# Performance work log

Hardware: AMD Instinct MI355X
Metric: run time of the kernel (lower is better)

Reference implementation:

```python
import jax, jax.numpy as jnp
import numpy as np

B, C, H, W = 4, 64, 128, 128
NUM_HEAD = 1
SCALE = (C // NUM_HEAD) ** (-0.5)


def setup_inputs():
    key = jax.random.key(0)
    ks = jax.random.split(key, 32)
    def nrm(k, shape, s=0.05):
        return jax.random.normal(k, shape, jnp.float32) * s
    inp = {"x": jax.random.normal(ks[0], (B, C, H, W), jnp.float32)}
    i = 1
    for wn, bn in [("Wq", "bq"), ("Wk", "bk"), ("Wv", "bv"), ("Wl", "bl"), ("Wo", "bo"), ("Wp", "bp")]:
        inp[wn] = nrm(ks[i], (C, C)); i += 1
        inp[bn] = nrm(ks[i], (C,)); i += 1
    inp["sch_dw"] = nrm(ks[i], (C, 1, 5, 1)); i += 1
    inp["sch_dwb"] = nrm(ks[i], (C,)); i += 1
    inp["sch_pw"] = nrm(ks[i], (C, C, 1, 1)); i += 1
    inp["sch_pwb"] = nrm(ks[i], (C,)); i += 1
    inp["scv_dw"] = nrm(ks[i], (C, 1, 1, 5)); i += 1
    inp["scv_dwb"] = nrm(ks[i], (C,)); i += 1
    inp["scv_pw"] = nrm(ks[i], (C, C, 1, 1)); i += 1
    inp["scv_pwb"] = nrm(ks[i], (C,)); i += 1
    inp["convh_w"] = nrm(ks[i], (C, C, 1, 1)); i += 1
    inp["convh_b"] = nrm(ks[i], (C,)); i += 1
    inp["dsc_dw"] = nrm(ks[i], (C, 1, 3, 3)); i += 1
    inp["dsc_dwb"] = nrm(ks[i], (C,)); i += 1
    inp["dsc_pw"] = nrm(ks[i], (C, C, 1, 1)); i += 1
    inp["dsc_pwb"] = nrm(ks[i], (C,)); i += 1
    inp["ln_g"] = jnp.ones((C,), jnp.float32)
    inp["ln_b"] = jnp.zeros((C,), jnp.float32)
    return inp


def _linear(x, w, b):  # x [B,N,C], w [C,C] (torch Linear convention: y = x @ w.T + b)
    return x @ w.T + b


def _dwconv(x, w, b, pad):  # depthwise: x [B,C,H,W], w [C,1,kh,kw]
    y = jax.lax.conv_general_dilated(x, w, (1, 1), [(pad[0], pad[0]), (pad[1], pad[1])],
                                     dimension_numbers=("NCHW", "OIHW", "NCHW"),
                                     feature_group_count=x.shape[1])
    return y + b[None, :, None, None]


def _pwconv(x, w, b):  # 1x1 conv: w [Co,Ci,1,1]
    return jnp.einsum("bchw,oc->bohw", x, w[:, :, 0, 0]) + b[None, :, None, None]


def _attn(q, k, v):  # [B,N,C] each; dense NxN softmax attention
    a = jax.nn.softmax(jnp.einsum("bnc,bmc->bnm", q, k) * SCALE, axis=-1)
    return jnp.einsum("bnm,bmc->bnc", a, v)


def _up2_bilinear(x):  # bilinear, scale 2, align_corners=True
    Bb, Cc, Hh, Ww = x.shape
    def coords(n):
        s = jnp.linspace(0.0, n - 1.0, 2 * n)
        i0 = jnp.floor(s).astype(jnp.int32)
        i1 = jnp.minimum(i0 + 1, n - 1)
        return i0, i1, (s - i0).astype(x.dtype)
    y0, y1, wy = coords(Hh)
    x0, x1, wx = coords(Ww)
    r = x[:, :, y0, :] * (1.0 - wy)[None, None, :, None] + x[:, :, y1, :] * wy[None, None, :, None]
    return r[:, :, :, x0] * (1.0 - wx) + r[:, :, :, x1] * wx


def _forward(x, Wq, bq, Wk, bk, Wv, bv, Wl, bl, Wo, bo, Wp, bp,
             sch_dw, sch_dwb, sch_pw, sch_pwb, scv_dw, scv_dwb, scv_pw, scv_pwb,
             convh_w, convh_b, dsc_dw, dsc_dwb, dsc_pw, dsc_pwb, ln_g, ln_b):
    Bb, Cc, Hh, Ww = x.shape
    # AvgPool2d(2,2)
    xp = x.reshape(Bb, Cc, Hh // 2, 2, Ww // 2, 2).mean((3, 5))
    Hp, Wp_ = Hh // 2, Ww // 2
    N = Hp * Wp_
    # forward_lpg: GAP-gated self-attention producing low-freq prompt
    gap = xp.mean((2, 3), keepdims=True)
    xg = (gap * xp).reshape(Bb, Cc, N).transpose(0, 2, 1)  # [B,N,C]
    q = _linear(xg, Wq, bq); k = _linear(xg, Wk, bk); v = _linear(xg, Wv, bv)
    prompt_l = _linear(_attn(q, k, v), Wl, bl).transpose(0, 2, 1).reshape(Bb, Cc, Hp, Wp_)
    # forward_hpg: separable strip-conv branches -> high-freq prompt
    x_h = _pwconv(jax.nn.gelu(_dwconv(xp, sch_dw, sch_dwb, (2, 0)), approximate=False), sch_pw, sch_pwb)
    x_v = _pwconv(jax.nn.gelu(_dwconv(xp, scv_dw, scv_dwb, (0, 2)), approximate=False), scv_pw, scv_pwb)
    prompt_h = _pwconv(x_h + x_v, convh_w, convh_b)
    # forward_pgc: cross-attention Q=high, K=low, V=linear(x)
    x_V = _linear(xp.reshape(Bb, Cc, N).transpose(0, 2, 1), Wo, bo)
    x_K = prompt_l.reshape(Bb, Cc, N).transpose(0, 2, 1)
    x_Q = prompt_h.reshape(Bb, Cc, N).transpose(0, 2, 1)
    prompt = _attn(x_Q, x_K, x_V)
    prompt = _linear(prompt, Wp, bp) + x_V
    # LayerNorm over channel dim
    mu = prompt.mean(-1, keepdims=True)
    var = jnp.mean((prompt - mu) ** 2, axis=-1, keepdims=True)
    p_norm = (prompt - mu) / jnp.sqrt(var + 1e-5) * ln_g + ln_b
    p_norm = p_norm.transpose(0, 2, 1).reshape(Bb, Cc, Hp, Wp_)
    # dsc: depthwise 3x3 -> GELU -> 1x1, residual
    out = _pwconv(jax.nn.gelu(_dwconv(p_norm, dsc_dw, dsc_dwb, (1, 1)), approximate=False), dsc_pw, dsc_pwb) + p_norm
    return _up2_bilinear(out)


def reference(x, Wq, bq, Wk, bk, Wv, bv, Wl, bl, Wo, bo, Wp, bp,
              sch_dw, sch_dwb, sch_pw, sch_pwb, scv_dw, scv_dwb, scv_pw, scv_pwb,
              convh_w, convh_b, dsc_dw, dsc_dwb, dsc_pw, dsc_pwb, ln_g, ln_b):
    return _forward(x, Wq, bq, Wk, bk, Wv, bv, Wl, bl, Wo, bo, Wp, bp,
                    sch_dw, sch_dwb, sch_pw, sch_pwb, scv_dw, scv_dwb, scv_pw, scv_pwb,
                    convh_w, convh_b, dsc_dw, dsc_dwb, dsc_pw, dsc_pwb, ln_g, ln_b)
```

## Files before the change

### kernel.cpp

```cpp
#include <hip/hip_runtime.h>
#include <math.h>

#define Bn 4
#define Cn 64
#define Np 4096
#define NSPLIT 8
#define SCALE2 0.18033688011112042f

typedef unsigned short ushort_t;
typedef __attribute__((ext_vector_type(4))) float f32x4;
typedef __attribute__((ext_vector_type(8))) short bf16x8;
typedef __attribute__((ext_vector_type(4))) short bf16x4;

__device__ __forceinline__ float gelu_exact(float x) {
    return 0.5f * x * (1.0f + erff(x * 0.70710678118654752440f));
}
__device__ __forceinline__ ushort_t f2bf(float f) {
    unsigned int u = __float_as_uint(f);
    u += 0x7fffu + ((u >> 16) & 1u);
    return (ushort_t)(u >> 16);
}
__device__ __forceinline__ ushort_t f2bf_tr(float f) {
    return (ushort_t)(__float_as_uint(f) >> 16);
}
__device__ __forceinline__ float bf2f(ushort_t h) {
    return __uint_as_float(((unsigned int)h) << 16);
}
__device__ __forceinline__ void gload_lds16(const ushort_t* g, ushort_t* l) {
    __builtin_amdgcn_global_load_lds(
        (const __attribute__((address_space(1))) void*)g,
        (__attribute__((address_space(3))) void*)l, 16, 0, 0);
}
__device__ __forceinline__ bf16x8 cvt8(const float v[8]) {
    bf16x8 r;
    #pragma unroll
    for (int j = 0; j < 8; ++j) r[j] = (short)f2bf(v[j]);
    return r;
}
__device__ __forceinline__ void gemm16b(const bf16x8 af[2], const ushort_t* __restrict__ Wb,
                                        int l16, int quad, f32x4* acc) {
    #pragma unroll
    for (int cb = 0; cb < 4; ++cb) {
        #pragma unroll
        for (int ks = 0; ks < 2; ++ks) {
            bf16x8 bw = *(const bf16x8*)(Wb + (cb * 16 + l16) * 64 + ks * 32 + quad * 8);
            acc[cb] = __builtin_amdgcn_mfma_f32_16x16x32_bf16(af[ks], bw, acc[cb], 0, 0, 0);
        }
    }
}
__device__ __forceinline__ void gemm16Tb(const bf16x8 af[2], const ushort_t* __restrict__ Wb,
                                         int l16, int quad, f32x4* acc) {
    #pragma unroll
    for (int cb = 0; cb < 4; ++cb) {
        #pragma unroll
        for (int ks = 0; ks < 2; ++ks) {
            bf16x8 bw = *(const bf16x8*)(Wb + (cb * 16 + l16) * 64 + ks * 32 + quad * 8);
            acc[cb] = __builtin_amdgcn_mfma_f32_16x16x32_bf16(bw, af[ks], acc[cb], 0, 0, 0);
        }
    }
}
__device__ __forceinline__ void aload(const float* xs, int row, int quad, bf16x8 af[2]) {
    #pragma unroll
    for (int ks = 0; ks < 2; ++ks) {
        float v[8];
        #pragma unroll
        for (int j = 0; j < 8; ++j) v[j] = xs[(ks * 32 + quad * 8 + j) * 65 + row];
        af[ks] = cvt8(v);
    }
}
__device__ __forceinline__ void stage_bchw(const float* __restrict__ X, int b, int n0, int t,
                                           float* xs) {
    #pragma unroll
    for (int u = 0; u < 16; ++u) {
        int idx = t + u * 256;
        int c = idx >> 6, nl = idx & 63;
        xs[c * 65 + nl] = X[((size_t)(b * Cn + c)) * Np + n0 + nl];
    }
}
__device__ __forceinline__ void stage_comb(const ushort_t* __restrict__ OpB, const float* linv,
                                           int b, int n0, int t, float* xs) {
    const size_t SS = (size_t)Bn * Np * Cn;
    int c4 = (t & 15) * 4;
    #pragma unroll
    for (int u = 0; u < 4; ++u) {
        int nl = (t >> 4) + u * 16;
        size_t gi = ((size_t)(b * Np + n0 + nl)) * Cn + c4;
        float s0 = 0.f, s1 = 0.f, s2 = 0.f, s3 = 0.f;
        #pragma unroll
        for (int sp = 0; sp < NSPLIT; ++sp) {
            ushort4 a = *(const ushort4*)(OpB + (size_t)sp * SS + gi);
            s0 += bf2f(a.x); s1 += bf2f(a.y); s2 += bf2f(a.z); s3 += bf2f(a.w);
        }
        float li = linv[nl];
        xs[(c4 + 0) * 65 + nl] = s0 * li;
        xs[(c4 + 1) * 65 + nl] = s1 * li;
        xs[(c4 + 2) * 65 + nl] = s2 * li;
        xs[(c4 + 3) * 65 + nl] = s3 * li;
    }
}
__device__ __forceinline__ void store_bnc_T(ushort_t* __restrict__ Y, int b, int n, int quad,
                                            const f32x4* acc, const float* __restrict__ bias,
                                            float mult) {
    #pragma unroll
    for (int cb = 0; cb < 4; ++cb) {
        int o0 = cb * 16 + quad * 4;
        ushort4 pk;
        pk.x = f2bf((acc[cb][0] + bias[o0 + 0]) * mult);
        pk.y = f2bf((acc[cb][1] + bias[o0 + 1]) * mult);
        pk.z = f2bf((acc[cb][2] + bias[o0 + 2]) * mult);
        pk.w = f2bf((acc[cb][3] + bias[o0 + 3]) * mult);
        *(ushort4*)(Y + ((size_t)(b * Np + n)) * Cn + o0) = pk;
    }
}
__device__ __forceinline__ void store_bchw_bf16(ushort_t* __restrict__ Y, int b, int nb, int l16,
                                                const f32x4* acc, const float* __restrict__ bias) {
    #pragma unroll
    for (int cb = 0; cb < 4; ++cb) {
        int col = cb * 16 + l16;
        float bb = bias[col];
        ushort4 pk;
        pk.x = f2bf(acc[cb][0] + bb); pk.y = f2bf(acc[cb][1] + bb);
        pk.z = f2bf(acc[cb][2] + bb); pk.w = f2bf(acc[cb][3] + bb);
        *(ushort4*)(Y + ((size_t)(b * Cn + col)) * Np + nb) = pk;
    }
}

__global__ void avgpool_kernel(const float* __restrict__ x, float* __restrict__ xp,
                               float* __restrict__ gap4k,
                               const float* __restrict__ convh_w, const float* __restrict__ convh_b,
                               const float* __restrict__ sch_pw, const float* __restrict__ sch_pwb,
                               const float* __restrict__ scv_pw, const float* __restrict__ scv_pwb,
                               ushort_t* __restrict__ Wc1b, ushort_t* __restrict__ Wc2b,
                               float* __restrict__ bcv,
                               const float* __restrict__ Wq, const float* __restrict__ Wk,
                               const float* __restrict__ Wv, const float* __restrict__ Wo,
                               const float* __restrict__ Wl, const float* __restrict__ Wp,
                               const float* __restrict__ dscpw, ushort_t* __restrict__ Wball) {
    if (blockIdx.x < 4096) {
        int idx = blockIdx.x * 256 + threadIdx.x;
        int j  = idx & 63;
        int i  = (idx >> 6) & 63;
        int bc = idx >> 12;
        const float* p = x + ((size_t)bc * 128 + 2 * i) * 128 + 2 * j;
        float v = 0.25f * (p[0] + p[1] + p[128] + p[129]);
        xp[idx] = v;
        float s = v;
        #pragma unroll
        for (int off = 1; off < 64; off <<= 1) s += __shfl_xor(s, off, 64);
        __shared__ float sm[4];
        if ((threadIdx.x & 63) == 0) sm[threadIdx.x >> 6] = s;
        __syncthreads();
        if (threadIdx.x == 0) gap4k[blockIdx.x] = sm[0] + sm[1] + sm[2] + sm[3];
    } else if (blockIdx.x < 4128) {
        int g = (blockIdx.x - 4096) * 256 + threadIdx.x;
        int sel = g >> 12, idx = g & 4095;
        int o = idx >> 6, c = idx & 63;
        const float* pw = sel ? scv_pw : sch_pw;
        float acc = 0.f;
        #pragma unroll 8
        for (int m = 0; m < 64; ++m) acc += convh_w[o * 64 + m] * pw[m * 64 + c];
        (sel ? Wc2b : Wc1b)[idx] = f2bf(acc * SCALE2);
        if (g < 64) {
            float ab = convh_b[g];
            for (int m = 0; m < 64; ++m) ab += convh_w[g * 64 + m] * (sch_pwb[m] + scv_pwb[m]);
            bcv[g] = ab * SCALE2;
        }
    } else {
        int g = (blockIdx.x - 4128) * 256 + threadIdx.x;
        int which = g >> 12, idx = g & 4095;
        const float* srcs[7] = {Wq, Wk, Wv, Wo, Wl, Wp, dscpw};
        Wball[g] = f2bf(srcs[which][idx]);
    }
}

__global__ __launch_bounds__(256) void qkv_dw_kernel(
    const float* __restrict__ xp, const float* __restrict__ gap4k,
    const ushort_t* __restrict__ Wqb, const float* __restrict__ bq,
    const ushort_t* __restrict__ Wkb, const float* __restrict__ bk,
    const ushort_t* __restrict__ Wvb, const float* __restrict__ bv,
    const ushort_t* __restrict__ Wob, const float* __restrict__ bo,
    ushort_t* __restrict__ qb, ushort_t* __restrict__ kb, ushort_t* __restrict__ vb,
    float* __restrict__ xV, ushort_t* __restrict__ xVtb,
    const float* __restrict__ wv5, const float* __restrict__ bv5,
    const float* __restrict__ wh5, const float* __restrict__ bh5,
    ushort_t* __restrict__ gh, ushort_t* __restrict__ gv) {
    int b = blockIdx.y, t = threadIdx.x;
    if (blockIdx.x >= 64) {
        int part = blockIdx.x - 64;
        int e = part * 1024 + t * 4;
        size_t base = (size_t)b * (Cn * Np) + e;
        int c = e >> 12, i = (e >> 6) & 63, j = e & 63;
        const float* p = xp + ((size_t)(b * Cn + c)) * Np;
        float accV[4], accH[4];
        #pragma unroll
        for (int k = 0; k < 4; ++k) { accV[k] = bv5[c]; accH[k] = bh5[c]; }
        #pragma unroll
        for (int d = 0; d < 5; ++d) {
            int ii = i + d - 2;
            if (ii >= 0 && ii < 64) {
                f32x4 r = *(const f32x4*)(p + ii * 64 + j);
                float w = wv5[c * 5 + d];
                accV[0] += w * r[0]; accV[1] += w * r[1];
                accV[2] += w * r[2]; accV[3] += w * r[3];
            }
        }
        f32x4 c0 = *(const f32x4*)(p + i * 64 + j);
        float col[8];
        col[2] = c0[0]; col[3] = c0[1]; col[4] = c0[2]; col[5] = c0[3];
        col[0] = (j >= 2)     ? p[i * 64 + j - 2] : 0.f;
        col[1] = (j >= 1)     ? p[i * 64 + j - 1] : 0.f;
        col[6] = (j + 4 < 64) ? p[i * 64 + j + 4] : 0.f;
        col[7] = (j + 5 < 64) ? p[i * 64 + j + 5] : 0.f;
        #pragma unroll
        for (int k = 0; k < 4; ++k) {
            #pragma unroll
            for (int d = 0; d < 5; ++d) accH[k] += wh5[c * 5 + d] * col[k + d];
        }
        ushort4 ph, pv_;
        ph.x = f2bf(gelu_exact(accV[0])); ph.y = f2bf(gelu_exact(accV[1]));
        ph.z = f2bf(gelu_exact(accV[2])); ph.w = f2bf(gelu_exact(accV[3]));
        pv_.x = f2bf(gelu_exact(accH[0])); pv_.y = f2bf(gelu_exact(accH[1]));
        pv_.z = f2bf(gelu_exact(accH[2])); pv_.w = f2bf(gelu_exact(accH[3]));
        *(ushort4*)(gh + base) = ph;
        *(ushort4*)(gv + base) = pv_;
        return;
    }
    __shared__ float xs[64 * 65];
    __shared__ float gl[64];
    int n0 = blockIdx.x * 64;
    int wv_ = t >> 6, lane = t & 63, l16 = lane & 15, quad = lane >> 4;
    stage_bchw(xp, b, n0, t, xs);
    if (t < 64) {
        float s = 0.f;
        #pragma unroll
        for (int u = 0; u < 16; ++u) s += gap4k[(b * 64 + t) * 16 + u];
        gl[t] = s * (1.f / 4096.f);
    }
    __syncthreads();
    int row = wv_ * 16 + l16;
    int n   = n0 + wv_ * 16 + l16;
    int nb  = n0 + wv_ * 16 + quad * 4;
    bf16x8 ar[2], ag[2];
    #pragma unroll
    for (int ks = 0; ks < 2; ++ks) {
        float vr[8], vg[8];
        #pragma unroll
        for (int j = 0; j < 8; ++j) {
            int k = ks * 32 + quad * 8 + j;
            float xv = xs[k * 65 + row];
            vr[j] = xv; vg[j] = xv * gl[k];
        }
        ar[ks] = cvt8(vr); ag[ks] = cvt8(vg);
    }
    f32x4 acc[4];
    #pragma unroll
    for (int cb = 0; cb < 4; ++cb) acc[cb] = (f32x4){0.f, 0.f, 0.f, 0.f};
    gemm16Tb(ag, Wqb, l16, quad, acc);
    store_bnc_T(qb, b, n, quad, acc, bq, SCALE2);
    #pragma unroll
    for (int cb = 0; cb < 4; ++cb) acc[cb] = (f32x4){0.f, 0.f, 0.f, 0.f};
    gemm16Tb(ag, Wkb, l16, quad, acc);
    store_bnc_T(kb, b, n, quad, acc, bk, 1.f);
    #pragma unroll
    for (int cb = 0; cb < 4; ++cb) acc[cb] = (f32x4){0.f, 0.f, 0.f, 0.f};
    gemm16b(ag, Wvb, l16, quad, acc);
    store_bchw_bf16(vb, b, nb, l16, acc, bv);
    #pragma unroll
    for (int cb = 0; cb < 4; ++cb) acc[cb] = (f32x4){0.f, 0.f, 0.f, 0.f};
    gemm16b(ar, Wob, l16, quad, acc);
    #pragma unroll
    for (int cb = 0; cb < 4; ++cb) {
        int col = cb * 16 + l16;
        float bb = bo[col];
        ushort4 pk;
        float y0 = acc[cb][0] + bb, y1 = acc[cb][1] + bb, y2 = acc[cb][2] + bb, y3 = acc[cb][3] + bb;
        xV[((size_t)(b * Np + nb + 0)) * Cn + col] = y0;
        xV[((size_t)(b * Np + nb + 1)) * Cn + col] = y1;
        xV[((size_t)(b * Np + nb + 2)) * Cn + col] = y2;
        xV[((size_t)(b * Np + nb + 3)) * Cn + col] = y3;
        pk.x = f2bf(y0); pk.y = f2bf(y1); pk.z = f2bf(y2); pk.w = f2bf(y3);
        *(ushort4*)(xVtb + ((size_t)(b * Cn + col)) * Np + nb) = pk;
    }
}

__device__ __forceinline__ void attn_wave(
    int wid, int b, const ushort_t* __restrict__ Qb, const ushort_t* __restrict__ Kb,
    const ushort_t* __restrict__ Vtb, ushort_t* __restrict__ OpB, float* __restrict__ Lpart,
    ushort_t* lds ) {
    int split = wid >> 7;
    int qt    = wid & 127;
    int n0    = qt * 32;
    int lane  = threadIdx.x & 63;
    int l16   = lane & 15, quad = lane >> 4;
    int kvbase = split * (Np / NSPLIT);

    const ushort_t* qp = Qb + ((size_t)(b * Np) + n0 + l16) * Cn + quad * 8;
    bf16x8 aq00 = *(const bf16x8*)(qp);
    bf16x8 aq01 = *(const bf16x8*)(qp + 32);
    bf16x8 aq10 = *(const bf16x8*)(qp + 16 * Cn);
    bf16x8 aq11 = *(const bf16x8*)(qp + 16 * Cn + 32);
    asm volatile("s_waitcnt vmcnt(0)" ::: "memory");

    f32x4 oa0[4], oa1[4];
    float psum0 = 0.f, psum1 = 0.f;
    #pragma unroll
    for (int db = 0; db < 4; ++db) {
        oa0[db] = (f32x4){0.f, 0.f, 0.f, 0.f};
        oa1[db] = (f32x4){0.f, 0.f, 0.f, 0.f};
    }

    const ushort_t* gK = Kb + ((size_t)b * Np + kvbase + (lane >> 3)) * Cn
                            + (((lane & 7) ^ (lane >> 3)) * 8);
    const ushort_t* gV = Vtb + ((size_t)(b * Cn) + (lane >> 1)) * Np + kvbase
                             + (((lane & 1) ^ ((lane >> 3) & 1)) * 8);
    ushort_t* kl = lds;
    ushort_t* vl = lds + 2048;

    const ushort_t* kr0 = lds + l16 * 64 + ((quad      ^ (l16 & 7))) * 8;
    const ushort_t* kr1 = lds + l16 * 64 + (((quad + 4) ^ (l16 & 7))) * 8;
    const ushort_t* vrb = lds + 2048 + l16 * 16
                        + (((quad >> 1) ^ ((l16 >> 2) & 1)) * 8) + (quad & 1) * 4;

    auto stage = [&](int buf) {
        ushort_t* kd = kl + buf * 1024;
        gload_lds16(gK,       kd);
        gload_lds16(gK + 512, kd + 512);
        ushort_t* vd = vl + buf * 1024;
        gload_lds16(gV,                   vd);
        gload_lds16(gV + (size_t)32 * Np, vd + 512);
        gK += 16 * Cn;
        gV += 16;
    };

    auto compute = [&](int ko) {
        bf16x8 k0 = *(const bf16x8*)(kr0 + ko);
        bf16x8 k1 = *(const bf16x8*)(kr1 + ko);
        f32x4 sa0 = (f32x4){0.f, 0.f, 0.f, 0.f};
        f32x4 sa1 = (f32x4){0.f, 0.f, 0.f, 0.f};
        __builtin_amdgcn_s_setprio(1);
        sa0 = __builtin_amdgcn_mfma_f32_16x16x32_bf16(k0, aq00, sa0, 0, 0, 0);
        sa0 = __builtin_amdgcn_mfma_f32_16x16x32_bf16(k1, aq01, sa0, 0, 0, 0);
        sa1 = __builtin_amdgcn_mfma_f32_16x16x32_bf16(k0, aq10, sa1, 0, 0, 0);
        sa1 = __builtin_amdgcn_mfma_f32_16x16x32_bf16(k1, aq11, sa1, 0, 0, 0);
        __builtin_amdgcn_s_setprio(0);
        float p0 = exp2f(sa0[0]), p1 = exp2f(sa0[1]), p2 = exp2f(sa0[2]), p3 = exp2f(sa0[3]);
        psum0 += (p0 + p1) + (p2 + p3);
        bf16x4 pb0;
        pb0[0] = (short)f2bf_tr(p0); pb0[1] = (short)f2bf_tr(p1);
        pb0[2] = (short)f2bf_tr(p2); pb0[3] = (short)f2bf_tr(p3);
        float q0 = exp2f(sa1[0]), q1 = exp2f(sa1[1]), q2 = exp2f(sa1[2]), q3 = exp2f(sa1[3]);
        psum1 += (q0 + q1) + (q2 + q3);
        bf16x4 pb1;
        pb1[0] = (short)f2bf_tr(q0); pb1[1] = (short)f2bf_tr(q1);
        pb1[2] = (short)f2bf_tr(q2); pb1[3] = (short)f2bf_tr(q3);
        __builtin_amdgcn_s_setprio(1);
        #pragma unroll
        for (int db = 0; db < 4; ++db) {
            bf16x4 av = *(const bf16x4*)(vrb + ko + db * 256);
            oa0[db] = __builtin_amdgcn_mfma_f32_16x16x16bf16_1k(av, pb0, oa0[db], 0, 0, 0);
            oa1[db] = __builtin_amdgcn_mfma_f32_16x16x16bf16_1k(av, pb1, oa1[db], 0, 0, 0);
        }
        __builtin_amdgcn_s_setprio(0);
    };

    const int NT = (Np / NSPLIT) / 16;
    stage(0);
    #pragma unroll 1
    for (int mm = 0; mm < NT / 2; ++mm) {
        stage(1);
        asm volatile("s_waitcnt vmcnt(4)" ::: "memory");
        compute(0);
        if (mm < NT / 2 - 1) {
            stage(0);
            asm volatile("s_waitcnt vmcnt(4)" ::: "memory");
        } else {
            asm volatile("s_waitcnt vmcnt(0)" ::: "memory");
        }
        compute(1024);
    }

    psum0 += __shfl_xor(psum0, 16, 64);
    psum0 += __shfl_xor(psum0, 32, 64);
    psum1 += __shfl_xor(psum1, 16, 64);
    psum1 += __shfl_xor(psum1, 32, 64);
    size_t obase = ((size_t)(split * Bn + b)) * Np;
    int n = n0 + l16;
    if (quad == 0) {
        Lpart[obase + n]      = psum0;
        Lpart[obase + n + 16] = psum1;
    }
    #pragma unroll
    for (int db = 0; db < 4; ++db) {
        ushort4 pk;
        pk.x = f2bf(oa0[db][0]); pk.y = f2bf(oa0[db][1]);
        pk.z = f2bf(oa0[db][2]); pk.w = f2bf(oa0[db][3]);
        *(ushort4*)(OpB + (obase + n) * Cn + db * 16 + quad * 4) = pk;
        ushort4 qk;
        qk.x = f2bf(oa1[db][0]); qk.y = f2bf(oa1[db][1]);
        qk.z = f2bf(oa1[db][2]); qk.w = f2bf(oa1[db][3]);
        *(ushort4*)(OpB + (obase + n + 16) * Cn + db * 16 + quad * 4) = qk;
    }
}

__device__ __forceinline__ void hpg_body(
    int tile, int b, const ushort_t* __restrict__ gh, const ushort_t* __restrict__ gv,
    const ushort_t* __restrict__ Wc1b, const ushort_t* __restrict__ Wc2b,
    const float* __restrict__ bcv,
    ushort_t* __restrict__ xQb, ushort_t* smem) {
    ushort_t* xs1 = smem;
    ushort_t* xs2 = smem + 4608;
    int n0 = tile * 64, t = threadIdx.x;
    int wv_ = t >> 6, lane = t & 63, l16 = lane & 15, quad = lane >> 4;
    #pragma unroll
    for (int u = 0; u < 4; ++u) {
        int lin = u * 256 + t;
        int c = lin >> 4, nl4 = (lin & 15) * 4;
        size_t gi = ((size_t)(b * Cn + c)) * Np + n0 + nl4;
        ushort4 g1 = *(const ushort4*)(gh + gi);
        ushort4 g2 = *(const ushort4*)(gv + gi);
        xs1[(nl4 + 0) * 72 + c] = g1.x; xs1[(nl4 + 1) * 72 + c] = g1.y;
        xs1[(nl4 + 2) * 72 + c] = g1.z; xs1[(nl4 + 3) * 72 + c] = g1.w;
        xs2[(nl4 + 0) * 72 + c] = g2.x; xs2[(nl4 + 1) * 72 + c] = g2.y;
        xs2[(nl4 + 2) * 72 + c] = g2.z; xs2[(nl4 + 3) * 72 + c] = g2.w;
    }
    __syncthreads();
    int row = wv_ * 16 + l16;
    bf16x8 a1[2], a2[2];
    #pragma unroll
    for (int ks = 0; ks < 2; ++ks) {
        a1[ks] = *(const bf16x8*)(xs1 + row * 72 + ks * 32 + quad * 8);
        a2[ks] = *(const bf16x8*)(xs2 + row * 72 + ks * 32 + quad * 8);
    }
    f32x4 acc[4];
    #pragma unroll
    for (int cb = 0; cb < 4; ++cb) acc[cb] = (f32x4){0.f, 0.f, 0.f, 0.f};
    gemm16Tb(a1, Wc1b, l16, quad, acc);
    gemm16Tb(a2, Wc2b, l16, quad, acc);
    store_bnc_T(xQb, b, n0 + wv_ * 16 + l16, quad, acc, bcv, 1.f);
}

__global__ __launch_bounds__(256) void attn_hpg_kernel(
    const ushort_t* __restrict__ Qb, const ushort_t* __restrict__ Kb,
    const ushort_t* __restrict__ Vtb, ushort_t* __restrict__ OpB, float* __restrict__ Lpart,
    const ushort_t* __restrict__ gh, const ushort_t* __restrict__ gv,
    const ushort_t* __restrict__ Wc1b, const ushort_t* __restrict__ Wc2b,
    const float* __restrict__ bcv, ushort_t* __restrict__ xQb) {
    __shared__ ushort_t smem[16384];
    int b = blockIdx.y;
    if (blockIdx.x < 256) {
        int wave = threadIdx.x >> 6;
        attn_wave(blockIdx.x * 4 + wave, b, Qb, Kb, Vtb, OpB, Lpart, smem + wave * 4096);
    } else {
        hpg_body(blockIdx.x - 256, b, gh, gv, Wc1b, Wc2b, bcv, xQb, smem);
    }
}

__global__ __launch_bounds__(256) void wl_mfma(
    const ushort_t* __restrict__ OpB, const float* __restrict__ Lp,
    const ushort_t* __restrict__ Wlb, const float* __restrict__ bl, ushort_t* __restrict__ xKb) {
    __shared__ float xs[64 * 65];
    __shared__ float linv[64];
    int b = blockIdx.y, n0 = blockIdx.x * 64, t = threadIdx.x;
    int wv_ = t >> 6, lane = t & 63, l16 = lane & 15, quad = lane >> 4;
    if (t < 64) {
        size_t li = (size_t)b * Np + n0 + t;
        const size_t LS = (size_t)Bn * Np;
        float s = 0.f;
        #pragma unroll
        for (int sp = 0; sp < NSPLIT; ++sp) s += Lp[(size_t)sp * LS + li];
        linv[t] = 1.f / s;
    }
    __syncthreads();
    stage_comb(OpB, linv, b, n0, t, xs);
    __syncthreads();
    bf16x8 af[2];
    aload(xs, wv_ * 16 + l16, quad, af);
    f32x4 acc[4];
    #pragma unroll
    for (int cb = 0; cb < 4; ++cb) acc[cb] = (f32x4){0.f, 0.f, 0.f, 0.f};
    gemm16Tb(af, Wlb, l16, quad, acc);
    store_bnc_T(xKb, b, n0 + wv_ * 16 + l16, quad, acc, bl, 1.f);
}

__global__ __launch_bounds__(256) void linln_mfma(
    const ushort_t* __restrict__ OpB, const float* __restrict__ Lp,
    const ushort_t* __restrict__ Wpb, const float* __restrict__ bp,
    const float* __restrict__ xV, const float* __restrict__ g, const float* __restrict__ beta,
    float* __restrict__ out) {
    __shared__ float xs[64 * 65];
    __shared__ float linv[64];
    int b = blockIdx.y, n0 = blockIdx.x * 64, t = threadIdx.x;
    int wv_ = t >> 6, lane = t & 63, l16 = lane & 15, quad = lane >> 4;
    if (t < 64) {
        size_t li = (size_t)b * Np + n0 + t;
        const size_t LS = (size_t)Bn * Np;
        float s = 0.f;
        #pragma unroll
        for (int sp = 0; sp < NSPLIT; ++sp) s += Lp[(size_t)sp * LS + li];
        linv[t] = 1.f / s;
    }
    __syncthreads();
    stage_comb(OpB, linv, b, n0, t, xs);
    __syncthreads();
    bf16x8 af[2];
    aload(xs, wv_ * 16 + l16, quad, af);
    f32x4 acc[4];
    #pragma unroll
    for (int cb = 0; cb < 4; ++cb) acc[cb] = (f32x4){0.f, 0.f, 0.f, 0.f};
    gemm16b(af, Wpb, l16, quad, acc);
    int nb = n0 + wv_ * 16 + quad * 4;
    float vals[4][4], gc[4], bec[4];
    #pragma unroll
    for (int cb = 0; cb < 4; ++cb) {
        int col = cb * 16 + l16;
        float bb = bp[col];
        gc[cb] = g[col]; bec[cb] = beta[col];
        #pragma unroll
        for (int r = 0; r < 4; ++r)
            vals[cb][r] = acc[cb][r] + bb + xV[((size_t)(b * Np + nb + r)) * Cn + col];
    }
    f32x4 yn[4];
    #pragma unroll
    for (int r = 0; r < 4; ++r) {
        float s = 0.f, s2 = 0.f;
        #pragma unroll
        for (int cb = 0; cb < 4; ++cb) { s += vals[cb][r]; s2 += vals[cb][r] * vals[cb][r]; }
        #pragma unroll
        for (int off = 1; off < 16; off <<= 1) {
            s  += __shfl_xor(s, off, 64);
            s2 += __shfl_xor(s2, off, 64);
        }
        float mu  = s * (1.f / 64.f);
        float var = s2 * (1.f / 64.f) - mu * mu;
        float ivs = rsqrtf(var + 1e-5f);
        #pragma unroll
        for (int cb = 0; cb < 4; ++cb)
            yn[cb][r] = (vals[cb][r] - mu) * ivs * gc[cb] + bec[cb];
    }
    #pragma unroll
    for (int cb = 0; cb < 4; ++cb)
        *(f32x4*)(out + ((size_t)(b * Cn + cb * 16 + l16)) * Np + nb) = yn[cb];
}

__global__ __launch_bounds__(256) void dsc_mfma(
    const float* __restrict__ X, const float* __restrict__ dw, const float* __restrict__ dwb,
    const ushort_t* __restrict__ Wb, const float* __restrict__ bias, float* __restrict__ out) {
    __shared__ float xs[64 * 65];
    int b = blockIdx.y, irow = blockIdx.x, n0 = irow * 64, t = threadIdx.x;
    int wv_ = t >> 6, lane = t & 63, l16 = lane & 15, quad = lane >> 4;
    int j = t & 63;
    #pragma unroll
    for (int u = 0; u < 16; ++u) {
        int c = (t >> 6) + u * 4;
        const float* p = X + ((size_t)(b * Cn + c)) * Np + n0;
        float acc = dwb[c];
        #pragma unroll
        for (int dy = 0; dy < 3; ++dy) {
            int ii = irow + dy - 1;
            if (ii < 0 || ii >= 64) continue;
            const float* pr = p + (dy - 1) * 64;
            #pragma unroll
            for (int dx = 0; dx < 3; ++dx) {
                int jj = j + dx - 1;
                if (jj < 0 || jj >= 64) continue;
                acc += dw[c * 9 + dy * 3 + dx] * pr[jj];
            }
        }
        xs[c * 65 + j] = gelu_exact(acc);
    }
    __syncthreads();
    bf16x8 af[2];
    aload(xs, wv_ * 16 + l16, quad, af);
    f32x4 acc[4];
    #pragma unroll
    for (int cb = 0; cb < 4; ++cb) acc[cb] = (f32x4){0.f, 0.f, 0.f, 0.f};
    gemm16b(af, Wb, l16, quad, acc);
    int nb = n0 + wv_ * 16 + quad * 4;
    #pragma unroll
    for (int cb = 0; cb < 4; ++cb) {
        int col = cb * 16 + l16;
        float bb = bias[col];
        size_t oi = ((size_t)(b * Cn + col)) * Np + nb;
        f32x4 rv = *(const f32x4*)(X + oi);
        f32x4 v4;
        #pragma unroll
        for (int r = 0; r < 4; ++r) v4[r] = acc[cb][r] + bb + rv[r];
        *(f32x4*)(out + oi) = v4;
    }
}

__global__ void upsample_kernel(const float* __restrict__ in, float* __restrict__ out) {
    int idx = blockIdx.x * 256 + threadIdx.x;
    int x4 = (idx & 31) * 4;
    int y  = (idx >> 5) & 127;
    int bc = idx >> 12;
    float sy = y * (63.f / 127.f);
    int y0 = (int)sy;
    float fy = sy - y0;
    int y1 = min(y0 + 1, 63);
    const float* p0 = in + (size_t)bc * Np + y0 * 64;
    const float* p1 = in + (size_t)bc * Np + y1 * 64;
    f32x4 o;
    #pragma unroll
    for (int k = 0; k < 4; ++k) {
        int xo = x4 + k;
        float sx = xo * (63.f / 127.f);
        int x0 = (int)sx;
        float fx = sx - x0;
        int x1 = min(x0 + 1, 63);
        float r0 = p0[x0] + (p0[x1] - p0[x0]) * fx;
        float r1 = p1[x0] + (p1[x1] - p1[x0]) * fx;
        o[k] = r0 + (r1 - r0) * fy;
    }
    *(f32x4*)(out + (size_t)idx * 4) = o;
}

extern "C" void kernel_launch(void* const* d_in, const int* in_sizes, int n_in,
                              void* d_out, int out_size, void* d_ws, size_t ws_size,
                              hipStream_t stream) {
    const float* x       = (const float*)d_in[0];
    const float* Wq      = (const float*)d_in[1];
    const float* bq      = (const float*)d_in[2];
    const float* Wk      = (const float*)d_in[3];
    const float* bk      = (const float*)d_in[4];
    const float* Wv      = (const float*)d_in[5];
    const float* bv      = (const float*)d_in[6];
    const float* Wl      = (const float*)d_in[7];
    const float* bl      = (const float*)d_in[8];
    const float* Wo      = (const float*)d_in[9];
    const float* bo      = (const float*)d_in[10];
    const float* Wp      = (const float*)d_in[11];
    const float* bp      = (const float*)d_in[12];
    const float* sch_dw  = (const float*)d_in[13];
    const float* sch_dwb = (const float*)d_in[14];
    const float* sch_pw  = (const float*)d_in[15];
    const float* sch_pwb = (const float*)d_in[16];
    const float* scv_dw  = (const float*)d_in[17];
    const float* scv_dwb = (const float*)d_in[18];
    const float* scv_pw  = (const float*)d_in[19];
    const float* scv_pwb = (const float*)d_in[20];
    const float* convh_w = (const float*)d_in[21];
    const float* convh_b = (const float*)d_in[22];
    const float* dsc_dw  = (const float*)d_in[23];
    const float* dsc_dwb = (const float*)d_in[24];
    const float* dsc_pw  = (const float*)d_in[25];
    const float* dsc_pwb = (const float*)d_in[26];
    const float* ln_g    = (const float*)d_in[27];
    const float* ln_b    = (const float*)d_in[28];

    float* ws = (float*)d_ws;
    const size_t SZ = (size_t)Bn * Np * Cn;
    float* xp   = ws;
    float* xV   = ws + SZ;
    ushort_t* ghb = (ushort_t*)(ws + 2 * SZ);
    ushort_t* gh  = ghb;
    ushort_t* gv  = ghb + SZ;
    float* f2   = ws + 2 * SZ;
    ushort_t* bws  = (ushort_t*)(ws + 3 * SZ);
    ushort_t* qb   = bws;
    ushort_t* kb_  = bws + SZ;
    ushort_t* vb   = bws + 2 * SZ;
    ushort_t* xKb  = bws + 3 * SZ;
    ushort_t* xVtb = bws + 4 * SZ;
    ushort_t* xQb  = bws + 5 * SZ;
    ushort_t* OpB  = (ushort_t*)(ws + 6 * SZ);
    float* gap4k  = ws + 10 * SZ;
    float* Lpart  = gap4k + 4096;
    float* wcslot = Lpart + (size_t)NSPLIT * Bn * Np;
    ushort_t* Wc1b = (ushort_t*)wcslot;
    ushort_t* Wc2b = Wc1b + 4096;
    float* bcv  = wcslot + 4096;
    ushort_t* Wball = (ushort_t*)(bcv + 64);
    ushort_t* Wqb   = Wball;
    ushort_t* Wkb   = Wball + 4096;
    ushort_t* Wvb   = Wball + 8192;
    ushort_t* Wob   = Wball + 12288;
    ushort_t* Wlb   = Wball + 16384;
    ushort_t* Wpb   = Wball + 20480;
    ushort_t* Wdscb = Wball + 24576;

    dim3 g64(64, Bn);

    avgpool_kernel<<<4096 + 32 + 112, 256, 0, stream>>>(x, xp, gap4k,
                                                  convh_w, convh_b, sch_pw, sch_pwb,
                                                  scv_pw, scv_pwb, Wc1b, Wc2b, bcv,
                                                  Wq, Wk, Wv, Wo, Wl, Wp, dsc_pw, Wball);
    qkv_dw_kernel<<<dim3(64 + 256, Bn), 256, 0, stream>>>(
        xp, gap4k, Wqb, bq, Wkb, bk, Wvb, bv, Wob, bo,
        qb, kb_, vb, xV, xVtb, sch_dw, sch_dwb, scv_dw, scv_dwb, gh, gv);
    attn_hpg_kernel<<<dim3(256 + 64, Bn), 256, 0, stream>>>(
        qb, kb_, vb, OpB, Lpart, gh, gv, Wc1b, Wc2b, bcv, xQb);
    wl_mfma<<<g64, 256, 0, stream>>>(OpB, Lpart, Wlb, bl, xKb);
    attn_hpg_kernel<<<dim3(256, Bn), 256, 0, stream>>>(
        xQb, xKb, xVtb, OpB, Lpart, gh, gv, Wc1b, Wc2b, bcv, xQb);
    linln_mfma<<<g64, 256, 0, stream>>>(OpB, Lpart, Wpb, bp, xV, ln_g, ln_b, xp);
    dsc_mfma<<<g64, 256, 0, stream>>>(xp, dsc_dw, dsc_dwb, Wdscb, dsc_pwb, f2);
    upsample_kernel<<<4096, 256, 0, stream>>>(f2, (float*)d_out);
}
```

Baseline: 262.7 us.

## Triple-buffer attention K/V staging with register prefetch; split dsc depthwise into own kernel

The attention wave loop moves from double to triple LDS buffering. K/V fragments for the next tile are read into registers while the current tile is computed, so the LDS read latency should overlap with MFMA work. LDS per block grows from 32KB to 48KB, which may lower occupancy. Separately, the depthwise 3x3 + GELU stage of dsc is split out into its own elementwise kernel (writing into the xV buffer), leaving dsc_mfma to do only the pointwise GEMM plus residual; this adds a kernel launch and an extra round trip through global memory.

```diff
diff --git a/kernel.cpp b/kernel.cpp
--- a/kernel.cpp
+++ b/kernel.cpp
@@ -313,35 +313,38 @@
                             + (((lane & 7) ^ (lane >> 3)) * 8);
     const ushort_t* gV = Vtb + ((size_t)(b * Cn) + (lane >> 1)) * Np + kvbase
                              + (((lane & 1) ^ ((lane >> 3) & 1)) * 8);
-    ushort_t* kl = lds;
-    ushort_t* vl = lds + 2048;
 
     const ushort_t* kr0 = lds + l16 * 64 + ((quad      ^ (l16 & 7))) * 8;
     const ushort_t* kr1 = lds + l16 * 64 + (((quad + 4) ^ (l16 & 7))) * 8;
-    const ushort_t* vrb = lds + 2048 + l16 * 16
+    const ushort_t* vrb = lds + 1024 + l16 * 16
                         + (((quad >> 1) ^ ((l16 >> 2) & 1)) * 8) + (quad & 1) * 4;
 
-    auto stage = [&](int buf) {
-        ushort_t* kd = kl + buf * 1024;
+    auto stage = [&](int buf3) {
+        ushort_t* kd = lds + buf3 * 2048;
         gload_lds16(gK,       kd);
         gload_lds16(gK + 512, kd + 512);
-        ushort_t* vd = vl + buf * 1024;
+        ushort_t* vd = kd + 1024;
         gload_lds16(gV,                   vd);
         gload_lds16(gV + (size_t)32 * Np, vd + 512);
         gK += 16 * Cn;
         gV += 16;
     };
 
-    auto compute = [&](int ko) {
-        bf16x8 k0 = *(const bf16x8*)(kr0 + ko);
-        bf16x8 k1 = *(const bf16x8*)(kr1 + ko);
+    auto ldread = [&](int bo, bf16x8* kf, bf16x4* vf) {
+        kf[0] = *(const bf16x8*)(kr0 + bo);
+        kf[1] = *(const bf16x8*)(kr1 + bo);
+        #pragma unroll
+        for (int db = 0; db < 4; ++db) vf[db] = *(const bf16x4*)(vrb + bo + db * 256);
+    };
+
+    auto computeR = [&](const bf16x8* kf, const bf16x4* vf) {
         f32x4 sa0 = (f32x4){0.f, 0.f, 0.f, 0.f};
         f32x4 sa1 = (f32x4){0.f, 0.f, 0.f, 0.f};
         __builtin_amdgcn_s_setprio(1);
-        sa0 = __builtin_amdgcn_mfma_f32_16x16x32_bf16(k0, aq00, sa0, 0, 0, 0);
-        sa0 = __builtin_amdgcn_mfma_f32_16x16x32_bf16(k1, aq01, sa0, 0, 0, 0);
-        sa1 = __builtin_amdgcn_mfma_f32_16x16x32_bf16(k0, aq10, sa1, 0, 0, 0);
-        sa1 = __builtin_amdgcn_mfma_f32_16x16x32_bf16(k1, aq11, sa1, 0, 0, 0);
+        sa0 = __builtin_amdgcn_mfma_f32_16x16x32_bf16(kf[0], aq00, sa0, 0, 0, 0);
+        sa0 = __builtin_amdgcn_mfma_f32_16x16x32_bf16(kf[1], aq01, sa0, 0, 0, 0);
+        sa1 = __builtin_amdgcn_mfma_f32_16x16x32_bf16(kf[0], aq10, sa1, 0, 0, 0);
+        sa1 = __builtin_amdgcn_mfma_f32_16x16x32_bf16(kf[1], aq11, sa1, 0, 0, 0);
         __builtin_amdgcn_s_setprio(0);
         float p0 = exp2f(sa0[0]), p1 = exp2f(sa0[1]), p2 = exp2f(sa0[2]), p3 = exp2f(sa0[3]);
         psum0 += (p0 + p1) + (p2 + p3);
@@ -356,28 +359,38 @@
         __builtin_amdgcn_s_setprio(1);
         #pragma unroll
         for (int db = 0; db < 4; ++db) {
-            bf16x4 av = *(const bf16x4*)(vrb + ko + db * 256);
-            oa0[db] = __builtin_amdgcn_mfma_f32_16x16x16bf16_1k(av, pb0, oa0[db], 0, 0, 0);
-            oa1[db] = __builtin_amdgcn_mfma_f32_16x16x16bf16_1k(av, pb1, oa1[db], 0, 0, 0);
+            oa0[db] = __builtin_amdgcn_mfma_f32_16x16x16bf16_1k(vf[db], pb0, oa0[db], 0, 0, 0);
+            oa1[db] = __builtin_amdgcn_mfma_f32_16x16x16bf16_1k(vf[db], pb1, oa1[db], 0, 0, 0);
         }
         __builtin_amdgcn_s_setprio(0);
     };
 
     const int NT = (Np / NSPLIT) / 16;
+    bf16x8 kfA[2], kfB[2];
+    bf16x4 vfA[4], vfB[4];
     stage(0);
+    stage(1);
+    asm volatile("s_waitcnt vmcnt(4)" ::: "memory");
+    ldread(0, kfA, vfA);
     #pragma unroll 1
-    for (int mm = 0; mm < NT / 2; ++mm) {
-        stage(1);
-        asm volatile("s_waitcnt vmcnt(4)" ::: "memory");
-        compute(0);
-        if (mm < NT / 2 - 1) {
-            stage(0);
+    for (int mm = 0; mm < NT - 1; ++mm) {
+        int s = mm + 2;
+        if (s < NT) {
+            stage(s % 3);
             asm volatile("s_waitcnt vmcnt(4)" ::: "memory");
         } else {
             asm volatile("s_waitcnt vmcnt(0)" ::: "memory");
         }
-        compute(1024);
-    }
+        int bo = ((mm + 1) % 3) * 2048;
+        if (mm & 1) {
+            ldread(bo, kfA, vfA);
+            computeR(kfB, vfB);
+        } else {
+            ldread(bo, kfB, vfB);
+            computeR(kfA, vfA);
+        }
+    }
+    if ((NT - 1) & 1) computeR(kfB, vfB); else computeR(kfA, vfA);
 
     psum0 += __shfl_xor(psum0, 16, 64);
     psum0 += __shfl_xor(psum0, 32, 64);
@@ -445,11 +458,11 @@
     const ushort_t* __restrict__ gh, const ushort_t* __restrict__ gv,
     const ushort_t* __restrict__ Wc1b, const ushort_t* __restrict__ Wc2b,
     const float* __restrict__ bcv, ushort_t* __restrict__ xQb) {
-    __shared__ ushort_t smem[16384];
+    __shared__ ushort_t smem[24576];
     int b = blockIdx.y;
     if (blockIdx.x < 256) {
         int wave = threadIdx.x >> 6;
-        attn_wave(blockIdx.x * 4 + wave, b, Qb, Kb, Vtb, OpB, Lpart, smem + wave * 4096);
+        attn_wave(blockIdx.x * 4 + wave, b, Qb, Kb, Vtb, OpB, Lpart, smem + wave * 6144);
     } else {
         hpg_body(blockIdx.x - 256, b, gh, gv, Wc1b, Wc2b, bcv, xQb, smem);
     }
@@ -542,32 +555,33 @@
         *(f32x4*)(out + ((size_t)(b * Cn + cb * 16 + l16)) * Np + nb) = yn[cb];
 }
 
+__global__ void dw3x3_gelu_kernel(const float* __restrict__ xin, const float* __restrict__ w,
+                                  const float* __restrict__ bias, float* __restrict__ out) {
+    int idx = blockIdx.x * 256 + threadIdx.x;
+    int j = idx & 63, i = (idx >> 6) & 63, bc = idx >> 12, c = bc & 63;
+    const float* p = xin + (size_t)bc * Np;
+    float acc = bias[c];
+    #pragma unroll
+    for (int dy = 0; dy < 3; ++dy) {
+        int ii = i + dy - 1;
+        if (ii < 0 || ii >= 64) continue;
+        #pragma unroll
+        for (int dx = 0; dx < 3; ++dx) {
+            int jj = j + dx - 1;
+            if (jj < 0 || jj >= 64) continue;
+            acc += w[c * 9 + dy * 3 + dx] * p[ii * 64 + jj];
+        }
+    }
+    out[idx] = gelu_exact(acc);
+}
+
 __global__ __launch_bounds__(256) void dsc_mfma(
-    const float* __restrict__ X, const float* __restrict__ dw, const float* __restrict__ dwb,
-    const ushort_t* __restrict__ Wb, const float* __restrict__ bias, float* __restrict__ out) {
+    const float* __restrict__ X, const ushort_t* __restrict__ Wb, const float* __restrict__ bias,
+    const float* __restrict__ res, float* __restrict__ out) {
     __shared__ float xs[64 * 65];
-    int b = blockIdx.y, irow = blockIdx.x, n0 = irow * 64, t = threadIdx.x;
+    int b = blockIdx.y, n0 = blockIdx.x * 64, t = threadIdx.x;
     int wv_ = t >> 6, lane = t & 63, l16 = lane & 15, quad = lane >> 4;
-    int j = t & 63;
-    #pragma unroll
-    for (int u = 0; u < 16; ++u) {
-        int c = (t >> 6) + u * 4;
-        const float* p = X + ((size_t)(b * Cn + c)) * Np + n0;
-        float acc = dwb[c];
-        #pragma unroll
-        for (int dy = 0; dy < 3; ++dy) {
-            int ii = irow + dy - 1;
-            if (ii < 0 || ii >= 64) continue;
-            const float* pr = p + (dy - 1) * 64;
-            #pragma unroll
-            for (int dx = 0; dx < 3; ++dx) {
-                int jj = j + dx - 1;
-                if (jj < 0 || jj >= 64) continue;
-                acc += dw[c * 9 + dy * 3 + dx] * pr[jj];
-            }
-        }
-        xs[c * 65 + j] = gelu_exact(acc);
-    }
+    stage_bchw(X, b, n0, t, xs);
     __syncthreads();
     bf16x8 af[2];
     aload(xs, wv_ * 16 + l16, quad, af);
@@ -581,7 +595,7 @@
         int col = cb * 16 + l16;
         float bb = bias[col];
         size_t oi = ((size_t)(b * Cn + col)) * Np + nb;
-        f32x4 rv = *(const f32x4*)(X + oi);
+        f32x4 rv = *(const f32x4*)(res + oi);
         f32x4 v4;
         #pragma unroll
         for (int r = 0; r < 4; ++r) v4[r] = acc[cb][r] + bb + rv[r];
@@ -694,6 +708,7 @@
     attn_hpg_kernel<<<dim3(256, Bn), 256, 0, stream>>>(
         xQb, xKb, xVtb, OpB, Lpart, gh, gv, Wc1b, Wc2b, bcv, xQb);
     linln_mfma<<<g64, 256, 0, stream>>>(OpB, Lpart, Wpb, bp, xV, ln_g, ln_b, xp);
-    dsc_mfma<<<g64, 256, 0, stream>>>(xp, dsc_dw, dsc_dwb, Wdscb, dsc_pwb, f2);
+    dw3x3_gelu_kernel<<<4096, 256, 0, stream>>>(xp, dsc_dw, dsc_dwb, xV);
+    dsc_mfma<<<g64, 256, 0, stream>>>(xV, Wdscb, dsc_pwb, xp, f2);
     upsample_kernel<<<4096, 256, 0, stream>>>(f2, (float*)d_out);
 }
```

Result: slower. 295.3 us (+12.4%).
